# Kernel tuning notes

Measured on AMD Instinct MI355X. Metric: run time of the kernel, lower is better.

The kernel has to match this reference:

```python
import jax, jax.numpy as jnp
import numpy as np
import math

B, A, IN_C, OUT_C = 64, 128, 128, 64

def _l2norm(x, eps=1e-12):
    # matches F.normalize(dim=1) on 2D input: x / max(||x||_2, eps) along last dim
    n = jnp.sqrt(jnp.sum(x * x, axis=-1, keepdims=True))
    return x / jnp.maximum(n, eps)

def setup_inputs() -> dict:
    key = jax.random.key(0)
    ks = jax.random.split(key, 7)
    s = 1.0 / math.sqrt(IN_C)
    return {
        "features": jax.random.normal(ks[0], (B, IN_C, A), dtype=jnp.float32),
        "Wq": jax.random.uniform(ks[1], (OUT_C, IN_C), jnp.float32, -s, s),
        "bq": jax.random.uniform(ks[2], (OUT_C,), jnp.float32, -s, s),
        "Wk": jax.random.uniform(ks[3], (OUT_C, IN_C), jnp.float32, -s, s),
        "bk": jax.random.uniform(ks[4], (OUT_C,), jnp.float32, -s, s),
        "Wv": jax.random.uniform(ks[5], (OUT_C, IN_C), jnp.float32, -s, s),
        "bv": jax.random.uniform(ks[6], (OUT_C,), jnp.float32, -s, s),
    }

def reference(features, Wq, bq, Wk, bk, Wv, bv):
    b = features.shape[0]
    f = jnp.transpose(features, (0, 2, 1))          # (b, a, in_c)
    a = f.shape[1]
    q = f @ Wq.T + bq                               # (b, a, d)
    k = f @ Wk.T + bk
    v = f @ Wv.T + bv
    d = q.shape[-1]
    qf = q.reshape(-1, d)                           # (N, d), N = b*a
    kf = k.reshape(-1, d)
    vf = v.reshape(-1, d)
    att = jax.nn.softmax(qf @ kf.T / math.sqrt(d), axis=1)  # (N, N)
    qkv = att @ vf                                  # (N, d)
    qkv_n = _l2norm(qkv).reshape(b, a, d)
    v_n = _l2norm(vf).reshape(b, a, d)
    # sim_s[i,j] = (1/a) * sum_t v_n[i,t] . qkv_n[j,t]  (diagonal-trace over 'a')
    sim_s = jnp.einsum('bad,cad->bc', v_n, qkv_n) / a
    return sim_s
```

## Files before the change

### kernel.cpp

```cpp
#include <hip/hip_runtime.h>
#include <hip/hip_bf16.h>

#define NROW 8192
#define INC  128
#define OUTC 64

typedef __bf16 bf16x8 __attribute__((ext_vector_type(8)));
typedef __bf16 bf16x4 __attribute__((ext_vector_type(4)));
typedef short  s16x4  __attribute__((ext_vector_type(4)));
typedef float  f32x4  __attribute__((ext_vector_type(4)));

static __device__ __forceinline__ f32x4 mfma16(bf16x8 a, bf16x8 b, f32x4 c) {
    return __builtin_amdgcn_mfma_f32_16x16x32_bf16(a, b, c, 0, 0, 0);
}
static __device__ __forceinline__ f32x4 mfma1k(s16x4 a, s16x4 b, f32x4 c) {
    return __builtin_amdgcn_mfma_f32_16x16x16bf16_1k(a, b, c, 0, 0, 0);
}

static __device__ __forceinline__ bf16x8 cvt8(float4 lo, float4 hi) {
    bf16x8 r;
    r[0] = (__bf16)lo.x; r[1] = (__bf16)lo.y; r[2] = (__bf16)lo.z; r[3] = (__bf16)lo.w;
    r[4] = (__bf16)hi.x; r[5] = (__bf16)hi.y; r[6] = (__bf16)hi.z; r[7] = (__bf16)hi.w;
    return r;
}

__global__ __launch_bounds__(256) void proj_kernel(
    const float* __restrict__ feat,
    const float* __restrict__ Wq, const float* __restrict__ bq,
    const float* __restrict__ Wk, const float* __restrict__ bk,
    const float* __restrict__ Wv, const float* __restrict__ bv,
    __hip_bfloat16* __restrict__ qbf, __hip_bfloat16* __restrict__ kbf,
    __hip_bfloat16* __restrict__ vbf, __hip_bfloat16* __restrict__ vnb)
{
    __shared__ float slab[32 * 132];
    __shared__ float vbuf[32 * 66];
    __shared__ float invb[32];

    const int blk = blockIdx.x;
    const int mat = blk >> 8;
    const int b   = (blk >> 2) & 63;
    const int a0  = (blk & 3) * 32;
    const int r0  = b * 128 + a0;
    const float* fb = feat + (size_t)b * INC * 128;

    for (int i = threadIdx.x; i < 32 * 128; i += 256) {
        int c = i >> 5, a = i & 31;
        slab[a * 132 + c] = fb[c * 128 + a0 + a];
    }
    __syncthreads();

    const int w    = threadIdx.x >> 6;
    const int lane = threadIdx.x & 63;
    const int l16  = lane & 15;
    const int quad = lane >> 4;
    const int n0   = w * 16;

    const float* W    = (mat == 0) ? Wq : (mat == 1) ? Wk : Wv;
    const float* bias = (mat == 0) ? bq : (mat == 1) ? bk : bv;

    f32x4 acc[2] = {{0.f,0.f,0.f,0.f},{0.f,0.f,0.f,0.f}};
    #pragma unroll
    for (int kc = 0; kc < 4; ++kc) {
        const int k0 = kc * 32 + quad * 8;
        const float* wr = W + (n0 + l16) * INC + k0;
        bf16x8 bfr = cvt8(*(const float4*)wr, *(const float4*)(wr + 4));
        #pragma unroll
        for (int u = 0; u < 2; ++u) {
            const float* ar = slab + (u * 16 + l16) * 132 + k0;
            bf16x8 afr = cvt8(*(const float4*)ar, *(const float4*)(ar + 4));
            acc[u] = mfma16(afr, bfr, acc[u]);
        }
    }
    const float bl = bias[n0 + l16];

    if (mat < 2) {
        __hip_bfloat16* dst = mat ? kbf : qbf;
        #pragma unroll
        for (int u = 0; u < 2; ++u) {
            const int base = ((((r0 >> 4) + u) * 4 + w) << 8) + l16;
            #pragma unroll
            for (int r = 0; r < 4; ++r)
                dst[base + (quad * 4 + r) * 16] = __float2bfloat16(acc[u][r] + bl);
        }
    } else {
        #pragma unroll
        for (int u = 0; u < 2; ++u)
            #pragma unroll
            for (int r = 0; r < 4; ++r)
                vbuf[(u * 16 + quad * 4 + r) * 66 + n0 + l16] = acc[u][r] + bl;
        __syncthreads();
        const int rl = threadIdx.x >> 3;
        const int jj = threadIdx.x & 7;
        float ss = 0.f;
        #pragma unroll
        for (int i = 0; i < 8; ++i) {
            float x = vbuf[rl * 66 + jj * 8 + i];
            ss += x * x;
        }
        ss += __shfl_xor(ss, 1, 64);
        ss += __shfl_xor(ss, 2, 64);
        ss += __shfl_xor(ss, 4, 64);
        if (jj == 0) invb[rl] = rsqrtf(fmaxf(ss, 1e-24f));
        __syncthreads();
        float inv = invb[rl];
        bf16x8 vp;
        #pragma unroll
        for (int i = 0; i < 8; ++i)
            vp[i] = (__bf16)(vbuf[rl * 66 + jj * 8 + i] * inv);
        *(bf16x8*)(vnb + (size_t)(r0 + rl) * 64 + jj * 8) = vp;
        const int tl = threadIdx.x & 15;
        const int n  = (threadIdx.x >> 4) & 3;
        const int s_ = threadIdx.x >> 6;
        bf16x8 pack;
        #pragma unroll
        for (int j = 0; j < 8; ++j) {
            int key = s_ * 8 + j;
            pack[j] = (__bf16)(vbuf[key * 66 + n * 16 + tl] * invb[key]);
        }
        const int base = ((((r0 >> 4) + (s_ >> 1)) * 4 + n) << 8) + tl * 16 + (s_ & 1) * 8;
        *(bf16x8*)(vbf + base) = pack;
    }
}

__global__ __launch_bounds__(256) void attn_kernel(
    const __hip_bfloat16* __restrict__ qbf,
    const __hip_bfloat16* __restrict__ kbf,
    const __hip_bfloat16* __restrict__ vbf,
    float* __restrict__ Opart, float* __restrict__ lpart)
{
    __shared__ float ored[4][32][65];
    __shared__ float lred[4][32];

    const int qtile = blockIdx.x >> 1;
    const int bg    = blockIdx.x & 1;
    const int w     = threadIdx.x >> 6;
    const int lane  = threadIdx.x & 63;
    const int l16   = lane & 15;
    const int quad  = lane >> 4;
    const int r0    = qtile * 32;
    const int fo    = l16 * 16 + quad * 4;

    s16x4 qf[2][4];
    #pragma unroll
    for (int u = 0; u < 2; ++u)
        #pragma unroll
        for (int kc = 0; kc < 4; ++kc)
            qf[u][kc] = *(const s16x4*)(qbf + ((((r0 >> 4) + u) * 4 + kc) << 8) + fo);

    f32x4 of[2][4];
    float lp[2] = {0.f, 0.f};
    #pragma unroll
    for (int u = 0; u < 2; ++u)
        #pragma unroll
        for (int n = 0; n < 4; ++n)
            of[u][n] = (f32x4){0.f, 0.f, 0.f, 0.f};

    const float coef = 0.18033688011112042f;

    int ck = bg * 256 + w * 64;
    s16x4 kf[2][4];
    #pragma unroll
    for (int h = 0; h < 2; ++h)
        #pragma unroll
        for (int kc = 0; kc < 4; ++kc)
            kf[h][kc] = *(const s16x4*)(kbf + (((ck + h) * 4 + kc) << 8) + fo);

    #pragma unroll 1
    for (int it = 0; it < 32; ++it) {
        s16x4 vf[4][2];
        #pragma unroll
        for (int n = 0; n < 4; ++n)
            #pragma unroll
            for (int h = 0; h < 2; ++h)
                vf[n][h] = *(const s16x4*)(vbf + (((ck + h) * 4 + n) << 8) + fo);
        const int cn = (it < 31) ? ck + 2 : ck;
        s16x4 kn[2][4];
        #pragma unroll
        for (int h = 0; h < 2; ++h)
            #pragma unroll
            for (int kc = 0; kc < 4; ++kc)
                kn[h][kc] = *(const s16x4*)(kbf + (((cn + h) * 4 + kc) << 8) + fo);

        const f32x4 zero = (f32x4){0.f, 0.f, 0.f, 0.f};
        #pragma unroll
        for (int u = 0; u < 2; ++u) {
            f32x4 s0 = zero, s1 = zero;
            #pragma unroll
            for (int kc = 0; kc < 4; ++kc) {
                s0 = mfma1k(kf[0][kc], qf[u][kc], s0);
                s1 = mfma1k(kf[1][kc], qf[u][kc], s1);
            }
            union { bf16x4 v; s16x4 s; } pf0, pf1;
            #pragma unroll
            for (int r = 0; r < 4; ++r) {
                float p0 = exp2f(s0[r] * coef);
                float p1 = exp2f(s1[r] * coef);
                lp[u] += p0 + p1;
                pf0.v[r] = (__bf16)p0;
                pf1.v[r] = (__bf16)p1;
            }
            #pragma unroll
            for (int n = 0; n < 4; ++n) {
                of[u][n] = mfma1k(pf0.s, vf[n][0], of[u][n]);
                of[u][n] = mfma1k(pf1.s, vf[n][1], of[u][n]);
            }
        }
        #pragma unroll
        for (int h = 0; h < 2; ++h)
            #pragma unroll
            for (int kc = 0; kc < 4; ++kc)
                kf[h][kc] = kn[h][kc];
        ck += 2;
    }

    #pragma unroll
    for (int u = 0; u < 2; ++u) {
        float v = lp[u];
        v += __shfl_xor(v, 16, 64);
        v += __shfl_xor(v, 32, 64);
        lp[u] = v;
    }
    if (quad == 0) {
        lred[w][l16]      = lp[0];
        lred[w][16 + l16] = lp[1];
    }
    #pragma unroll
    for (int u = 0; u < 2; ++u)
        #pragma unroll
        for (int n = 0; n < 4; ++n)
            #pragma unroll
            for (int r = 0; r < 4; ++r)
                ored[w][u * 16 + quad * 4 + r][n * 16 + l16] = of[u][n][r];
    __syncthreads();

    const int task = blockIdx.x;
    float* Ob = Opart + (size_t)task * 2048;
    for (int e = threadIdx.x; e < 2048; e += 256) {
        const int row = e >> 6, col = e & 63;
        Ob[e] = ored[0][row][col] + ored[1][row][col]
              + ored[2][row][col] + ored[3][row][col];
    }
    if (threadIdx.x < 32)
        lpart[task * 32 + threadIdx.x] =
            lred[0][threadIdx.x] + lred[1][threadIdx.x]
          + lred[2][threadIdx.x] + lred[3][threadIdx.x];
}

__global__ __launch_bounds__(256) void combine_kernel(
    const float* __restrict__ Opart, const float* __restrict__ lpart,
    __hip_bfloat16* __restrict__ qnb)
{
    const int r    = blockIdx.x * 4 + (threadIdx.x >> 6);
    const int c    = threadIdx.x & 63;
    const int tile = r >> 5, row = r & 31;
    float acc = 0.f, lsum = 0.f;
    #pragma unroll
    for (int g = 0; g < 2; ++g) {
        int task = tile * 2 + g;
        acc  += Opart[(size_t)task * 2048 + row * 64 + c];
        lsum += lpart[task * 32 + row];
    }
    float q = acc / lsum;
    float ss = q * q;
    ss += __shfl_xor(ss, 1, 64);
    ss += __shfl_xor(ss, 2, 64);
    ss += __shfl_xor(ss, 4, 64);
    ss += __shfl_xor(ss, 8, 64);
    ss += __shfl_xor(ss, 16, 64);
    ss += __shfl_xor(ss, 32, 64);
    qnb[(size_t)r * 64 + c] = __float2bfloat16(q * rsqrtf(fmaxf(ss, 1e-24f)));
}

__global__ __launch_bounds__(64) void sim_kernel(
    const __hip_bfloat16* __restrict__ vnb,
    const __hip_bfloat16* __restrict__ qnb,
    float* __restrict__ out)
{
    const int lane = threadIdx.x;
    const int l16  = lane & 15;
    const int quad = lane >> 4;
    const int kblk = blockIdx.x * 256;

    f32x4 acc[4][4];
    #pragma unroll
    for (int mi = 0; mi < 4; ++mi)
        #pragma unroll
        for (int ni = 0; ni < 4; ++ni)
            acc[mi][ni] = (f32x4){0.f, 0.f, 0.f, 0.f};

    #pragma unroll
    for (int ks = 0; ks < 8; ++ks) {
        const int k0 = kblk + ks * 32 + quad * 8;
        bf16x8 af[4], bfv[4];
        #pragma unroll
        for (int mi = 0; mi < 4; ++mi)
            af[mi] = *(const bf16x8*)(vnb + (size_t)(mi * 16 + l16) * 8192 + k0);
        #pragma unroll
        for (int ni = 0; ni < 4; ++ni)
            bfv[ni] = *(const bf16x8*)(qnb + (size_t)(ni * 16 + l16) * 8192 + k0);
        #pragma unroll
        for (int mi = 0; mi < 4; ++mi)
            #pragma unroll
            for (int ni = 0; ni < 4; ++ni)
                acc[mi][ni] = mfma16(af[mi], bfv[ni], acc[mi][ni]);
    }

    #pragma unroll
    for (int mi = 0; mi < 4; ++mi)
        #pragma unroll
        for (int ni = 0; ni < 4; ++ni)
            #pragma unroll
            for (int r = 0; r < 4; ++r)
                atomicAdd(&out[(mi * 16 + quad * 4 + r) * 64 + ni * 16 + l16],
                          acc[mi][ni][r] * (1.f / 128.f));
}

extern "C" void kernel_launch(void* const* d_in, const int* in_sizes, int n_in,
                              void* d_out, int out_size, void* d_ws, size_t ws_size,
                              hipStream_t stream)
{
    const float* feat = (const float*)d_in[0];
    const float* Wq   = (const float*)d_in[1];
    const float* bq   = (const float*)d_in[2];
    const float* Wk   = (const float*)d_in[3];
    const float* bk   = (const float*)d_in[4];
    const float* Wv   = (const float*)d_in[5];
    const float* bv   = (const float*)d_in[6];
    float* out = (float*)d_out;

    const size_t MB = 1u << 20;
    char* ws = (char*)d_ws;
    __hip_bfloat16* qbf = (__hip_bfloat16*)(ws);
    __hip_bfloat16* kbf = (__hip_bfloat16*)(ws + 1 * MB);
    __hip_bfloat16* vbf = (__hip_bfloat16*)(ws + 2 * MB);
    __hip_bfloat16* vnb = (__hip_bfloat16*)(ws + 3 * MB);
    float* Opart = (float*)(ws + 4 * MB);
    float* lpart = (float*)(ws + 8 * MB);
    __hip_bfloat16* qnb = (__hip_bfloat16*)(ws + 9 * MB);

    (void)hipMemsetAsync(out, 0, 64 * 64 * sizeof(float), stream);
    proj_kernel<<<768, 256, 0, stream>>>(feat, Wq, bq, Wk, bk, Wv, bv, qbf, kbf, vbf, vnb);
    attn_kernel<<<512, 256, 0, stream>>>(qbf, kbf, vbf, Opart, lpart);
    combine_kernel<<<2048, 256, 0, stream>>>(Opart, lpart, qnb);
    sim_kernel<<<32, 64, 0, stream>>>(vnb, qnb, out);
}
```

Before: 124.9 us.

## Split attention key range across 8 blocks per query tile for more parallelism

The attention kernel now splits each 32-row query tile's keys across 8 blocks instead of 2, so it launches 2048 blocks, each running 8 iterations instead of 32. The intra-block reduction now uses half the shared memory: two waves write, then two waves accumulate in place. The combine kernel sums 8 partials instead of 2, and workspace offsets move to fit the larger partial buffer. This is meant to raise occupancy and fill the GPU's CUs better, at the cost of four times more partial-output traffic to global memory and a heavier combine step.

```diff
diff --git a/kernel.cpp b/kernel.cpp
--- a/kernel.cpp
+++ b/kernel.cpp
@@ -128,11 +128,11 @@
     const __hip_bfloat16* __restrict__ vbf,
     float* __restrict__ Opart, float* __restrict__ lpart)
 {
-    __shared__ float ored[4][32][65];
-    __shared__ float lred[4][32];
-
-    const int qtile = blockIdx.x >> 1;
-    const int bg    = blockIdx.x & 1;
+    __shared__ float ored[2][32][65];
+    __shared__ float lred[2][32];
+
+    const int qtile = blockIdx.x >> 3;
+    const int bg    = blockIdx.x & 7;
     const int w     = threadIdx.x >> 6;
     const int lane  = threadIdx.x & 63;
     const int l16   = lane & 15;
@@ -157,7 +157,7 @@
 
     const float coef = 0.18033688011112042f;
 
-    int ck = bg * 256 + w * 64;
+    int ck = bg * 64 + w * 16;
     s16x4 kf[2][4];
     #pragma unroll
     for (int h = 0; h < 2; ++h)
@@ -166,14 +166,14 @@
             kf[h][kc] = *(const s16x4*)(kbf + (((ck + h) * 4 + kc) << 8) + fo);
 
     #pragma unroll 1
-    for (int it = 0; it < 32; ++it) {
+    for (int it = 0; it < 8; ++it) {
         s16x4 vf[4][2];
         #pragma unroll
         for (int n = 0; n < 4; ++n)
             #pragma unroll
             for (int h = 0; h < 2; ++h)
                 vf[n][h] = *(const s16x4*)(vbf + (((ck + h) * 4 + n) << 8) + fo);
-        const int cn = (it < 31) ? ck + 2 : ck;
+        const int cn = (it < 7) ? ck + 2 : ck;
         s16x4 kn[2][4];
         #pragma unroll
         for (int h = 0; h < 2; ++h)
@@ -220,30 +220,45 @@
         v += __shfl_xor(v, 32, 64);
         lp[u] = v;
     }
-    if (quad == 0) {
-        lred[w][l16]      = lp[0];
-        lred[w][16 + l16] = lp[1];
-    }
-    #pragma unroll
-    for (int u = 0; u < 2; ++u)
-        #pragma unroll
-        for (int n = 0; n < 4; ++n)
-            #pragma unroll
-            for (int r = 0; r < 4; ++r)
-                ored[w][u * 16 + quad * 4 + r][n * 16 + l16] = of[u][n][r];
+
+    if (w >= 2) {
+        #pragma unroll
+        for (int u = 0; u < 2; ++u)
+            #pragma unroll
+            for (int n = 0; n < 4; ++n)
+                #pragma unroll
+                for (int r = 0; r < 4; ++r)
+                    ored[w - 2][u * 16 + quad * 4 + r][n * 16 + l16] = of[u][n][r];
+        if (quad == 0) {
+            lred[w - 2][l16]      = lp[0];
+            lred[w - 2][16 + l16] = lp[1];
+        }
+    }
     __syncthreads();
-
+    if (w < 2) {
+        #pragma unroll
+        for (int u = 0; u < 2; ++u)
+            #pragma unroll
+            for (int n = 0; n < 4; ++n)
+                #pragma unroll
+                for (int r = 0; r < 4; ++r) {
+                    float v = of[u][n][r] + ored[w][u * 16 + quad * 4 + r][n * 16 + l16];
+                    ored[w][u * 16 + quad * 4 + r][n * 16 + l16] = v;
+                }
+        if (quad == 0) {
+            lred[w][l16]      += lp[0];
+            lred[w][16 + l16] += lp[1];
+        }
+    }
+    __syncthreads();
     const int task = blockIdx.x;
     float* Ob = Opart + (size_t)task * 2048;
     for (int e = threadIdx.x; e < 2048; e += 256) {
         const int row = e >> 6, col = e & 63;
-        Ob[e] = ored[0][row][col] + ored[1][row][col]
-              + ored[2][row][col] + ored[3][row][col];
+        Ob[e] = ored[0][row][col] + ored[1][row][col];
     }
     if (threadIdx.x < 32)
-        lpart[task * 32 + threadIdx.x] =
-            lred[0][threadIdx.x] + lred[1][threadIdx.x]
-          + lred[2][threadIdx.x] + lred[3][threadIdx.x];
+        lpart[task * 32 + threadIdx.x] = lred[0][threadIdx.x] + lred[1][threadIdx.x];
 }
 
 __global__ __launch_bounds__(256) void combine_kernel(
@@ -255,8 +270,8 @@
     const int tile = r >> 5, row = r & 31;
     float acc = 0.f, lsum = 0.f;
     #pragma unroll
-    for (int g = 0; g < 2; ++g) {
-        int task = tile * 2 + g;
+    for (int g = 0; g < 8; ++g) {
+        int task = tile * 8 + g;
         acc  += Opart[(size_t)task * 2048 + row * 64 + c];
         lsum += lpart[task * 32 + row];
     }
@@ -335,12 +350,12 @@
     __hip_bfloat16* vbf = (__hip_bfloat16*)(ws + 2 * MB);
     __hip_bfloat16* vnb = (__hip_bfloat16*)(ws + 3 * MB);
     float* Opart = (float*)(ws + 4 * MB);
-    float* lpart = (float*)(ws + 8 * MB);
-    __hip_bfloat16* qnb = (__hip_bfloat16*)(ws + 9 * MB);
+    float* lpart = (float*)(ws + 20 * MB);
+    __hip_bfloat16* qnb = (__hip_bfloat16*)(ws + 21 * MB);
 
     (void)hipMemsetAsync(out, 0, 64 * 64 * sizeof(float), stream);
     proj_kernel<<<768, 256, 0, stream>>>(feat, Wq, bq, Wk, bk, Wv, bv, qbf, kbf, vbf, vnb);
-    attn_kernel<<<512, 256, 0, stream>>>(qbf, kbf, vbf, Opart, lpart);
+    attn_kernel<<<2048, 256, 0, stream>>>(qbf, kbf, vbf, Opart, lpart);
     combine_kernel<<<2048, 256, 0, stream>>>(Opart, lpart, qnb);
     sim_kernel<<<32, 64, 0, stream>>>(vnb, qnb, out);
 }
```

After: 132.6 us. +6.2%, slower.
